# Kernel tuning notes

Hardware: AMD Instinct MI355X
Metric: run time of the kernel (lower is better)

Reference implementation:

```python
import jax, jax.numpy as jnp
import numpy as np

B, T, D, H = 4, 1024, 1024, 16
DK = D // H
SCALE = float(np.sqrt(DK))


def setup_inputs() -> dict:
    key = jax.random.key(0)
    ks = jax.random.split(key, 12)
    std = 1.0 / np.sqrt(D)
    inp = {
        "x": jax.random.normal(ks[0], (B, T, D), dtype=jnp.float32),
        "s2_distances": jax.random.uniform(ks[1], (B, T, T), dtype=jnp.float32),
        # causal mask: 1 where attention allowed (j <= i)
        "mask": jnp.broadcast_to(jnp.tril(jnp.ones((T, T), dtype=jnp.int32)), (B, T, T)),
        "Wq": jax.random.uniform(ks[2], (D, D), jnp.float32, -std, std),
        "bq": jax.random.uniform(ks[3], (D,), jnp.float32, -std, std),
        "Wk": jax.random.uniform(ks[4], (D, D), jnp.float32, -std, std),
        "bk": jax.random.uniform(ks[5], (D,), jnp.float32, -std, std),
        "Wv": jax.random.uniform(ks[6], (D, D), jnp.float32, -std, std),
        "bv": jax.random.uniform(ks[7], (D,), jnp.float32, -std, std),
        "Wo": jax.random.uniform(ks[8], (D, D), jnp.float32, -std, std),
        "bo": jax.random.uniform(ks[9], (D,), jnp.float32, -std, std),
        "spatial_weight": jnp.float32(0.5),
    }
    return inp


def reference(x, s2_distances, mask, Wq, bq, Wk, bk, Wv, bv, Wo, bo, spatial_weight):
    b, t, _ = x.shape
    # projections: torch nn.Linear is x @ W.T + b
    def proj(W, bias):
        y = jnp.einsum("btd,ed->bte", x, W) + bias
        return y.reshape(b, t, H, DK).transpose(0, 2, 1, 3)  # [B,H,T,dk]

    Q, K, V = proj(Wq, bq), proj(Wk, bk), proj(Wv, bv)
    # scores: QK^T/sqrt(dk) - |alpha| * dist  (dist broadcast over heads)
    scores = jnp.einsum("bhqd,bhkd->bhqk", Q, K) / SCALE
    scores = scores - jnp.abs(spatial_weight) * s2_distances[:, None, :, :]
    scores = jnp.where(mask[:, None, :, :] == 0, -jnp.inf, scores)
    probs = jax.nn.softmax(scores, axis=-1)
    out = jnp.einsum("bhqk,bhkd->bhqd", probs, V)
    out = out.transpose(0, 2, 1, 3).reshape(b, t, D)
    return jnp.einsum("btd,ed->bte", out, Wo) + bo
```

## Files before the change

kernel.cpp:

```cpp
#include <hip/hip_runtime.h>
#include <stdint.h>

#define Tt 1024
#define Dd 1024
#define Hh 16

typedef unsigned short u16;
typedef __attribute__((ext_vector_type(8))) short short8;
typedef __attribute__((ext_vector_type(4))) float f32x4;
typedef __attribute__((ext_vector_type(4))) unsigned short u16x4;

typedef const __attribute__((address_space(1))) uint32_t* gptr_t;
typedef __attribute__((address_space(3))) uint32_t* lptr_t;

#define QSCALE 0.18033688011112042f
#define LOG2E 1.4426950408889634f

static __device__ __forceinline__ u16 f2bf(float f) {
  union { float f; unsigned u; } x;
  x.f = f;
  unsigned u = x.u;
  return (u16)((u + 0x7fffu + ((u >> 16) & 1u)) >> 16);
}

static __device__ __forceinline__ u16 f2bf_fast(float f) {
  union { float f; unsigned u; } x;
  x.f = f;
  return (u16)((x.u + 0x8000u) >> 16);
}

static __device__ __forceinline__ float fexp2(float x) {
#if __has_builtin(__builtin_amdgcn_exp2f)
  return __builtin_amdgcn_exp2f(x);
#else
  return exp2f(x);
#endif
}

__global__ __launch_bounds__(256) void cvt_kernel(
    const float* __restrict__ x, const float* __restrict__ wq,
    const float* __restrict__ wk, const float* __restrict__ wv,
    const float* __restrict__ wo, u16* __restrict__ xb, u16* __restrict__ wb) {
  size_t i = ((size_t)blockIdx.x * 256 + threadIdx.x) * 4;
  const size_t XN = (size_t)4 * 1024 * 1024;
  const float* src;
  u16* dst;
  size_t off;
  if (i < XN) {
    src = x; dst = xb; off = i;
  } else {
    size_t j = i - XN;
    int wi = (int)(j >> 20);
    src = (wi == 0) ? wq : (wi == 1) ? wk : (wi == 2) ? wv : wo;
    dst = wb + ((size_t)wi << 20);
    off = j & ((1u << 20) - 1);
  }
  float4 v = *(const float4*)(src + off);
  u16x4 o;
  o.x = f2bf(v.x); o.y = f2bf(v.y); o.z = f2bf(v.z); o.w = f2bf(v.w);
  *(u16x4*)(dst + off) = o;
}

static __device__ __forceinline__ void gemm_mainloop(
    const u16* __restrict__ A, const u16* __restrict__ W,
    u16* lA, u16* lB, int m0, int n0, f32x4 acc[4][4]) {
  const int t = threadIdx.x;
  const int w = t >> 6, l = t & 63;
  const int quad = l >> 4, l15 = l & 15;
  const int wm = (w >> 1) * 64, wn = (w & 1) * 64;
  const int srow = t >> 3;
  const int scol = (t & 7) * 8;
  const u16* ga = A + (size_t)(m0 + srow) * Dd + scol;
  const u16* gb = W + (size_t)(n0 + srow) * Dd + scol;
  char* lAc = (char*)lA;
  char* lBc = (char*)lB;
  const int lbase = w * 8 * 128;
  for (int k0 = 0; k0 < Dd; k0 += 64) {
    __syncthreads();
#pragma unroll
    for (int i = 0; i < 4; i++) {
      __builtin_amdgcn_global_load_lds((gptr_t)(ga + k0 + (size_t)i * 32 * Dd),
                                       (lptr_t)(lAc + lbase + i * 32 * 128), 16, 0, 0);
      __builtin_amdgcn_global_load_lds((gptr_t)(gb + k0 + (size_t)i * 32 * Dd),
                                       (lptr_t)(lBc + lbase + i * 32 * 128), 16, 0, 0);
    }
    __builtin_amdgcn_s_waitcnt(0);
    __syncthreads();
#pragma unroll
    for (int kk = 0; kk < 2; kk++) {
      short8 af[4], bfr[4];
#pragma unroll
      for (int mi = 0; mi < 4; mi++)
        af[mi] = *(const short8*)(lA + (wm + mi * 16 + l15) * 64 + kk * 32 + quad * 8);
#pragma unroll
      for (int ni = 0; ni < 4; ni++)
        bfr[ni] = *(const short8*)(lB + (wn + ni * 16 + l15) * 64 + kk * 32 + quad * 8);
#pragma unroll
      for (int mi = 0; mi < 4; mi++)
#pragma unroll
        for (int ni = 0; ni < 4; ni++)
          acc[mi][ni] = __builtin_amdgcn_mfma_f32_16x16x32_bf16(af[mi], bfr[ni], acc[mi][ni], 0, 0, 0);
    }
  }
}

__global__ __launch_bounds__(256) void gemm_qkv_kernel(
    const u16* __restrict__ xb, const u16* __restrict__ wb,
    const float* __restrict__ bq, const float* __restrict__ bk,
    const float* __restrict__ bv, u16* __restrict__ Q, u16* __restrict__ Kk,
    u16* __restrict__ Vt) {
  __shared__ u16 smem[128 * 128];
  u16* lA = smem;
  u16* lB = smem + 128 * 64;
  const int z = blockIdx.z;
  const u16* W = wb + ((size_t)z << 20);
  const float* bias = (z == 0) ? bq : (z == 1) ? bk : bv;
  const int m0 = blockIdx.x * 128, n0 = blockIdx.y * 128;
  f32x4 acc[4][4];
#pragma unroll
  for (int i = 0; i < 4; i++)
#pragma unroll
    for (int j = 0; j < 4; j++) acc[i][j] = (f32x4){0.f, 0.f, 0.f, 0.f};
  gemm_mainloop(xb, W, lA, lB, m0, n0, acc);
  const int t = threadIdx.x, w = t >> 6, l = t & 63, quad = l >> 4, l15 = l & 15;
  const int wm = (w >> 1) * 64, wn = (w & 1) * 64;
  __syncthreads();
  const float scl = (z == 0) ? QSCALE : 1.0f;
  if (z < 2) {
#pragma unroll
    for (int mi = 0; mi < 4; mi++)
#pragma unroll
      for (int ni = 0; ni < 4; ni++) {
        const int n = wn + ni * 16 + l15;
        const float bn = bias[n0 + n];
#pragma unroll
        for (int r = 0; r < 4; r++) {
          const int m = wm + mi * 16 + quad * 4 + r;
          smem[m * 128 + n] = f2bf((acc[mi][ni][r] + bn) * scl);
        }
      }
  } else {
#pragma unroll
    for (int mi = 0; mi < 4; mi++)
#pragma unroll
      for (int ni = 0; ni < 4; ni++) {
        const int n = wn + ni * 16 + l15;
        const float bn = bias[n0 + n];
        u16x4 o;
        o.x = f2bf(acc[mi][ni][0] + bn);
        o.y = f2bf(acc[mi][ni][1] + bn);
        o.z = f2bf(acc[mi][ni][2] + bn);
        o.w = f2bf(acc[mi][ni][3] + bn);
        *(u16x4*)&smem[n * 128 + wm + mi * 16 + quad * 4] = o;
      }
  }
  __syncthreads();
  const int row = t >> 4;
  const int col = (t & 15) * 8;
  if (z < 2) {
    u16* out = (z == 0) ? Q : Kk;
#pragma unroll
    for (int it = 0; it < 8; it++) {
      const int rr = it * 16 + row;
      *(short8*)(out + (size_t)(m0 + rr) * Dd + n0 + col) = *(const short8*)&smem[rr * 128 + col];
    }
  } else {
    const int b2 = m0 >> 10, tt0 = m0 & (Tt - 1);
#pragma unroll
    for (int it = 0; it < 8; it++) {
      const int rr = it * 16 + row;
      *(short8*)(Vt + ((size_t)b2 * Dd + n0 + rr) * Tt + tt0 + col) = *(const short8*)&smem[rr * 128 + col];
    }
  }
}

__global__ __launch_bounds__(256) void gemm_out_kernel(
    const u16* __restrict__ Ao, const u16* __restrict__ Wo,
    const float* __restrict__ bo, float* __restrict__ out) {
  __shared__ u16 lA[128 * 64];
  __shared__ u16 lB[128 * 64];
  const int m0 = blockIdx.x * 128, n0 = blockIdx.y * 128;
  f32x4 acc[4][4];
#pragma unroll
  for (int i = 0; i < 4; i++)
#pragma unroll
    for (int j = 0; j < 4; j++) acc[i][j] = (f32x4){0.f, 0.f, 0.f, 0.f};
  gemm_mainloop(Ao, Wo, lA, lB, m0, n0, acc);
  const int t = threadIdx.x, w = t >> 6, l = t & 63, quad = l >> 4, l15 = l & 15;
  const int wm = (w >> 1) * 64, wn = (w & 1) * 64;
#pragma unroll
  for (int mi = 0; mi < 4; mi++)
#pragma unroll
    for (int ni = 0; ni < 4; ni++) {
      const int n = n0 + wn + ni * 16 + l15;
      const float bn = bo[n];
#pragma unroll
      for (int r = 0; r < 4; r++) {
        const int m = m0 + wm + mi * 16 + quad * 4 + r;
        out[(size_t)m * Dd + n] = acc[mi][ni][r] + bn;
      }
    }
}

__global__ __launch_bounds__(256) void attn_kernel(
    const u16* __restrict__ Q, const u16* __restrict__ Kk,
    const u16* __restrict__ Vt, const float* __restrict__ dist,
    const float* __restrict__ alphap, u16* __restrict__ Oo) {
  __shared__ u16 lK[2][64 * 64];
  __shared__ u16 lV[2][64 * 64];
  __shared__ u16 lPp[4][16 * 64];
  const int t = threadIdx.x, w = t >> 6, l = t & 63, quad = l >> 4, l15 = l & 15;
  const int pi = blockIdx.x & 7;
  const int bh = blockIdx.x >> 3;
  const int h = bh & (Hh - 1), b = bh >> 4;
  const int qbA = pi, qbB = 15 - pi;
  const float aL = fabsf(alphap[0]) * LOG2E;
  const float* distb = dist + (size_t)b * Tt * Tt;

  const int srow = w * 8 + (l >> 3);
  const int schunk = ((l & 7) ^ ((l >> 3) & 7)) * 8;
  const u16* gK = Kk + ((size_t)b * Tt + srow) * Dd + h * 64 + schunk;
  const u16* gV = Vt + ((size_t)b * Dd + h * 64 + srow) * Tt + schunk;
  char* lKc0 = (char*)&lK[0][0];
  char* lVc0 = (char*)&lV[0][0];
  const int wbase = w * 1024;

  auto stage = [&](int k0, int buf) {
#pragma unroll
    for (int i = 0; i < 2; i++) {
      __builtin_amdgcn_global_load_lds(
          (gptr_t)(gK + (size_t)(k0 + i * 32) * Dd),
          (lptr_t)(lKc0 + buf * 8192 + wbase + i * 4096), 16, 0, 0);
      __builtin_amdgcn_global_load_lds(
          (gptr_t)(gV + (size_t)(i * 32) * Tt + k0),
          (lptr_t)(lVc0 + buf * 8192 + wbase + i * 4096), 16, 0, 0);
    }
  };

  const int qrowA = qbA * 64 + w * 16 + l15;
  const int qrowB = qbB * 64 + w * 16 + l15;
  const u16* QpA = Q + ((size_t)b * Tt + qrowA) * Dd + h * 64 + quad * 8;
  const u16* QpB = Q + ((size_t)b * Tt + qrowB) * Dd + h * 64 + quad * 8;
  const short8 qfA0 = *(const short8*)QpA;
  const short8 qfA1 = *(const short8*)(QpA + 32);
  const short8 qfB0 = *(const short8*)QpB;
  const short8 qfB1 = *(const short8*)(QpB + 32);
  const float* dpA = distb + (size_t)qrowA * Tt + quad * 4;
  const float* dpB = distb + (size_t)qrowB * Tt + quad * 4;

  const int xr = l15 & 7;
  u16* lpr = &lPp[w][l15 * 64];

  f32x4 ddA[4], ddB[4];
  stage(0, 0);
#pragma unroll
  for (int nt = 0; nt < 4; nt++) ddA[nt] = *(const f32x4*)(dpA + nt * 16);

  int gi = 0;
#pragma unroll 1
  for (int half = 0; half < 2; half++) {
    const int qb = half ? qbB : qbA;
    const int q0 = qb * 64;
    const int niter = qb + 1;
    const short8 qf0 = half ? qfB0 : qfA0;
    const short8 qf1 = half ? qfB1 : qfA1;
    const float* dp = half ? dpB : dpA;
    const int qrow = half ? qrowB : qrowA;
    f32x4 oacc[4];
#pragma unroll
    for (int dt = 0; dt < 4; dt++) oacc[dt] = (f32x4){0.f, 0.f, 0.f, 0.f};
    float lsum = 0.f;

#pragma unroll 1
    for (int kt = 0; kt < niter; kt++, gi++) {
      const int buf = gi & 1;
      __builtin_amdgcn_s_waitcnt(0);
      __syncthreads();
      const bool more = (kt + 1 < niter);
      if (more) {
        stage((kt + 1) * 64, buf ^ 1);
#pragma unroll
        for (int nt = 0; nt < 4; nt++)
          ddB[nt] = *(const f32x4*)(dp + (kt + 1) * 64 + nt * 16);
      } else if (half == 0) {
        stage(0, buf ^ 1);
#pragma unroll
        for (int nt = 0; nt < 4; nt++) ddB[nt] = *(const f32x4*)(dpB + nt * 16);
      }
      f32x4 sacc[4];
#pragma unroll
      for (int nt = 0; nt < 4; nt++) {
#pragma unroll
        for (int r = 0; r < 4; r++) sacc[nt][r] = -aL * ddA[nt][r];
      }
#pragma unroll
      for (int ks = 0; ks < 2; ks++) {
        const short8 qf = ks ? qf1 : qf0;
        const int cs = ((ks * 4 + quad) ^ xr) * 8;
#pragma unroll
        for (int nt = 0; nt < 4; nt++) {
          const short8 kf = *(const short8*)&lK[buf][(nt * 16 + l15) * 64 + cs];
          sacc[nt] = __builtin_amdgcn_mfma_f32_16x16x32_bf16(kf, qf, sacc[nt], 0, 0, 0);
        }
      }
      if (kt == qb) {
        const int kbase = kt * 64 + quad * 4;
#pragma unroll
        for (int nt = 0; nt < 4; nt++) {
          u16x4 pk;
#pragma unroll
          for (int r = 0; r < 4; r++) {
            const float p = (kbase + nt * 16 + r <= qrow) ? fexp2(sacc[nt][r]) : 0.f;
            lsum += p;
            pk[r] = f2bf_fast(p);
          }
          *(u16x4*)&lpr[((nt * 4 + quad) ^ (xr << 1)) * 4] = pk;
        }
      } else {
#pragma unroll
        for (int nt = 0; nt < 4; nt++) {
          u16x4 pk;
#pragma unroll
          for (int r = 0; r < 4; r++) {
            const float p = fexp2(sacc[nt][r]);
            lsum += p;
            pk[r] = f2bf_fast(p);
          }
          *(u16x4*)&lpr[((nt * 4 + quad) ^ (xr << 1)) * 4] = pk;
        }
      }
#pragma unroll
      for (int ks = 0; ks < 2; ks++) {
        const short8 pa = *(const short8*)&lpr[((ks * 4 + quad) ^ xr) * 8];
        const int cs = ((ks * 4 + quad) ^ xr) * 8;
#pragma unroll
        for (int dt = 0; dt < 4; dt++) {
          const short8 vf = *(const short8*)&lV[buf][(dt * 16 + l15) * 64 + cs];
          oacc[dt] = __builtin_amdgcn_mfma_f32_16x16x32_bf16(pa, vf, oacc[dt], 0, 0, 0);
        }
      }
#pragma unroll
      for (int nt = 0; nt < 4; nt++) ddA[nt] = ddB[nt];
    }

    lsum += __shfl_xor(lsum, 16);
    lsum += __shfl_xor(lsum, 32);
    const float inv = 1.0f / lsum;
    float invq[4];
#pragma unroll
    for (int r = 0; r < 4; r++) invq[r] = __shfl(inv, quad * 4 + r);
#pragma unroll
    for (int dt = 0; dt < 4; dt++) {
#pragma unroll
      for (int r = 0; r < 4; r++) {
        Oo[((size_t)b * Tt + q0 + w * 16 + quad * 4 + r) * Dd + h * 64 + dt * 16 + l15] =
            f2bf(oacc[dt][r] * invq[r]);
      }
    }
  }
}

extern "C" void kernel_launch(void* const* d_in, const int* in_sizes, int n_in,
                              void* d_out, int out_size, void* d_ws, size_t ws_size,
                              hipStream_t stream) {
  const float* x = (const float*)d_in[0];
  const float* dist = (const float*)d_in[1];
  const float* Wq = (const float*)d_in[3];
  const float* bq = (const float*)d_in[4];
  const float* Wk = (const float*)d_in[5];
  const float* bk = (const float*)d_in[6];
  const float* Wv = (const float*)d_in[7];
  const float* bv = (const float*)d_in[8];
  const float* Wo = (const float*)d_in[9];
  const float* bo = (const float*)d_in[10];
  const float* alphap = (const float*)d_in[11];

  char* ws = (char*)d_ws;
  u16* xb = (u16*)(ws);
  u16* wb = (u16*)(ws + ((size_t)8 << 20));
  u16* Qb = (u16*)(ws + ((size_t)16 << 20));
  u16* Kb = (u16*)(ws + ((size_t)24 << 20));
  u16* Vtb = (u16*)(ws + ((size_t)32 << 20));
  u16* Ob = xb;
  float* outp = (float*)d_out;

  cvt_kernel<<<8192, 256, 0, stream>>>(x, Wq, Wk, Wv, Wo, xb, wb);
  dim3 g1(32, 8, 3);
  gemm_qkv_kernel<<<g1, 256, 0, stream>>>(xb, wb, bq, bk, bv, Qb, Kb, Vtb);
  attn_kernel<<<512, 256, 0, stream>>>(Qb, Kb, Vtb, dist, alphap, Ob);
  dim3 g2(32, 8);
  gemm_out_kernel<<<g2, 256, 0, stream>>>(Ob, wb + ((size_t)3 << 20), bo, outp);
}
```

Before: 223.8 us.

## Double-buffer GEMM LDS tiles, swizzle LDS layout, use 512-thread blocks

The projection GEMM mainloop now double-buffers its LDS tiles, issuing the next k-slice's global-to-LDS loads before computing the current one, so only one barrier is needed per iteration. The LDS column index is XOR-swizzled to reduce bank conflicts on the MFMA fragment reads. Blocks grow to 8 waves, each computing a 32x64 sub-tile, which halves the per-thread accumulators and adds waves for latency hiding. The cost is 64KB of LDS per block, which may cap how many blocks fit on a CU.

```diff
diff --git a/kernel.cpp b/kernel.cpp
--- a/kernel.cpp
+++ b/kernel.cpp
@@ -61,42 +61,53 @@
   *(u16x4*)(dst + off) = o;
 }
 
-static __device__ __forceinline__ void gemm_mainloop(
+static __device__ __forceinline__ void gemm_mainloop_db(
     const u16* __restrict__ A, const u16* __restrict__ W,
-    u16* lA, u16* lB, int m0, int n0, f32x4 acc[4][4]) {
+    u16* lds, int m0, int n0, f32x4 acc[2][4]) {
   const int t = threadIdx.x;
   const int w = t >> 6, l = t & 63;
   const int quad = l >> 4, l15 = l & 15;
-  const int wm = (w >> 1) * 64, wn = (w & 1) * 64;
+  const int wm = (w >> 1) * 32, wn = (w & 1) * 64;
   const int srow = t >> 3;
-  const int scol = (t & 7) * 8;
+  const int scol = ((l & 7) ^ ((l >> 3) & 7)) * 8;
   const u16* ga = A + (size_t)(m0 + srow) * Dd + scol;
   const u16* gb = W + (size_t)(n0 + srow) * Dd + scol;
-  char* lAc = (char*)lA;
-  char* lBc = (char*)lB;
-  const int lbase = w * 8 * 128;
-  for (int k0 = 0; k0 < Dd; k0 += 64) {
-    __syncthreads();
-#pragma unroll
-    for (int i = 0; i < 4; i++) {
-      __builtin_amdgcn_global_load_lds((gptr_t)(ga + k0 + (size_t)i * 32 * Dd),
-                                       (lptr_t)(lAc + lbase + i * 32 * 128), 16, 0, 0);
-      __builtin_amdgcn_global_load_lds((gptr_t)(gb + k0 + (size_t)i * 32 * Dd),
-                                       (lptr_t)(lBc + lbase + i * 32 * 128), 16, 0, 0);
-    }
+  char* ldc = (char*)lds;
+  const int xr = l15 & 7;
+
+  auto stage = [&](int k0, int buf) {
+    char* base = ldc + buf * 32768 + w * 1024;
+#pragma unroll
+    for (int i = 0; i < 2; i++) {
+      __builtin_amdgcn_global_load_lds((gptr_t)(ga + k0 + (size_t)i * 64 * Dd),
+                                       (lptr_t)(base + i * 8192), 16, 0, 0);
+      __builtin_amdgcn_global_load_lds((gptr_t)(gb + k0 + (size_t)i * 64 * Dd),
+                                       (lptr_t)(base + 16384 + i * 8192), 16, 0, 0);
+    }
+  };
+
+  stage(0, 0);
+#pragma unroll 1
+  for (int it = 0; it < Dd / 64; it++) {
+    const int buf = it & 1;
     __builtin_amdgcn_s_waitcnt(0);
     __syncthreads();
+    if (it + 1 < Dd / 64) stage((it + 1) * 64, buf ^ 1);
+    const u16* lA = lds + buf * 16384;
+    const u16* lB = lA + 8192;
 #pragma unroll
     for (int kk = 0; kk < 2; kk++) {
-      short8 af[4], bfr[4];
-#pragma unroll
-      for (int mi = 0; mi < 4; mi++)
-        af[mi] = *(const short8*)(lA + (wm + mi * 16 + l15) * 64 + kk * 32 + quad * 8);
+      short8 af[2], bfr[4];
+#pragma unroll
+      for (int mi = 0; mi < 2; mi++)
+        af[mi] = *(const short8*)(lA + (wm + mi * 16 + l15) * 64 +
+                                  (((kk * 4 + quad) ^ xr) * 8));
 #pragma unroll
       for (int ni = 0; ni < 4; ni++)
-        bfr[ni] = *(const short8*)(lB + (wn + ni * 16 + l15) * 64 + kk * 32 + quad * 8);
-#pragma unroll
-      for (int mi = 0; mi < 4; mi++)
+        bfr[ni] = *(const short8*)(lB + (wn + ni * 16 + l15) * 64 +
+                                   (((kk * 4 + quad) ^ xr) * 8));
+#pragma unroll
+      for (int mi = 0; mi < 2; mi++)
 #pragma unroll
         for (int ni = 0; ni < 4; ni++)
           acc[mi][ni] = __builtin_amdgcn_mfma_f32_16x16x32_bf16(af[mi], bfr[ni], acc[mi][ni], 0, 0, 0);
@@ -104,31 +115,30 @@
   }
 }
 
-__global__ __launch_bounds__(256) void gemm_qkv_kernel(
+__global__ __launch_bounds__(512) void gemm_qkv_kernel(
     const u16* __restrict__ xb, const u16* __restrict__ wb,
     const float* __restrict__ bq, const float* __restrict__ bk,
     const float* __restrict__ bv, u16* __restrict__ Q, u16* __restrict__ Kk,
     u16* __restrict__ Vt) {
-  __shared__ u16 smem[128 * 128];
-  u16* lA = smem;
-  u16* lB = smem + 128 * 64;
+  __shared__ u16 lds[2 * 16384];
   const int z = blockIdx.z;
   const u16* W = wb + ((size_t)z << 20);
   const float* bias = (z == 0) ? bq : (z == 1) ? bk : bv;
   const int m0 = blockIdx.x * 128, n0 = blockIdx.y * 128;
-  f32x4 acc[4][4];
-#pragma unroll
-  for (int i = 0; i < 4; i++)
+  f32x4 acc[2][4];
+#pragma unroll
+  for (int i = 0; i < 2; i++)
 #pragma unroll
     for (int j = 0; j < 4; j++) acc[i][j] = (f32x4){0.f, 0.f, 0.f, 0.f};
-  gemm_mainloop(xb, W, lA, lB, m0, n0, acc);
+  gemm_mainloop_db(xb, W, lds, m0, n0, acc);
   const int t = threadIdx.x, w = t >> 6, l = t & 63, quad = l >> 4, l15 = l & 15;
-  const int wm = (w >> 1) * 64, wn = (w & 1) * 64;
+  const int wm = (w >> 1) * 32, wn = (w & 1) * 64;
+  u16* smem = lds;
   __syncthreads();
   const float scl = (z == 0) ? QSCALE : 1.0f;
   if (z < 2) {
 #pragma unroll
-    for (int mi = 0; mi < 4; mi++)
+    for (int mi = 0; mi < 2; mi++)
 #pragma unroll
       for (int ni = 0; ni < 4; ni++) {
         const int n = wn + ni * 16 + l15;
@@ -141,7 +151,7 @@
       }
   } else {
 #pragma unroll
-    for (int mi = 0; mi < 4; mi++)
+    for (int mi = 0; mi < 2; mi++)
 #pragma unroll
       for (int ni = 0; ni < 4; ni++) {
         const int n = wn + ni * 16 + l15;
@@ -160,36 +170,35 @@
   if (z < 2) {
     u16* out = (z == 0) ? Q : Kk;
 #pragma unroll
-    for (int it = 0; it < 8; it++) {
-      const int rr = it * 16 + row;
+    for (int it = 0; it < 4; it++) {
+      const int rr = it * 32 + row;
       *(short8*)(out + (size_t)(m0 + rr) * Dd + n0 + col) = *(const short8*)&smem[rr * 128 + col];
     }
   } else {
     const int b2 = m0 >> 10, tt0 = m0 & (Tt - 1);
 #pragma unroll
-    for (int it = 0; it < 8; it++) {
-      const int rr = it * 16 + row;
+    for (int it = 0; it < 4; it++) {
+      const int rr = it * 32 + row;
       *(short8*)(Vt + ((size_t)b2 * Dd + n0 + rr) * Tt + tt0 + col) = *(const short8*)&smem[rr * 128 + col];
     }
   }
 }
 
-__global__ __launch_bounds__(256) void gemm_out_kernel(
+__global__ __launch_bounds__(512) void gemm_out_kernel(
     const u16* __restrict__ Ao, const u16* __restrict__ Wo,
     const float* __restrict__ bo, float* __restrict__ out) {
-  __shared__ u16 lA[128 * 64];
-  __shared__ u16 lB[128 * 64];
+  __shared__ u16 lds[2 * 16384];
   const int m0 = blockIdx.x * 128, n0 = blockIdx.y * 128;
-  f32x4 acc[4][4];
-#pragma unroll
-  for (int i = 0; i < 4; i++)
+  f32x4 acc[2][4];
+#pragma unroll
+  for (int i = 0; i < 2; i++)
 #pragma unroll
     for (int j = 0; j < 4; j++) acc[i][j] = (f32x4){0.f, 0.f, 0.f, 0.f};
-  gemm_mainloop(Ao, Wo, lA, lB, m0, n0, acc);
+  gemm_mainloop_db(Ao, Wo, lds, m0, n0, acc);
   const int t = threadIdx.x, w = t >> 6, l = t & 63, quad = l >> 4, l15 = l & 15;
-  const int wm = (w >> 1) * 64, wn = (w & 1) * 64;
-#pragma unroll
-  for (int mi = 0; mi < 4; mi++)
+  const int wm = (w >> 1) * 32, wn = (w & 1) * 64;
+#pragma unroll
+  for (int mi = 0; mi < 2; mi++)
 #pragma unroll
     for (int ni = 0; ni < 4; ni++) {
       const int n = n0 + wn + ni * 16 + l15;
@@ -386,8 +395,8 @@
 
   cvt_kernel<<<8192, 256, 0, stream>>>(x, Wq, Wk, Wv, Wo, xb, wb);
   dim3 g1(32, 8, 3);
-  gemm_qkv_kernel<<<g1, 256, 0, stream>>>(xb, wb, bq, bk, bv, Qb, Kb, Vtb);
+  gemm_qkv_kernel<<<g1, 512, 0, stream>>>(xb, wb, bq, bk, bv, Qb, Kb, Vtb);
   attn_kernel<<<512, 256, 0, stream>>>(Qb, Kb, Vtb, dist, alphap, Ob);
   dim3 g2(32, 8);
-  gemm_out_kernel<<<g2, 256, 0, stream>>>(Ob, wb + ((size_t)3 << 20), bo, outp);
-}
+  gemm_out_kernel<<<g2, 512, 0, stream>>>(Ob, wb + ((size_t)3 << 20), bo, outp);
+}
```

After: 196.6 us. 1.14x faster.
